# Kernel tuning notes

Hardware: AMD Instinct MI355X
Metric: run time of the kernel (lower is better)

## Reference

```python
import jax, jax.numpy as jnp
import numpy as np

MARGIN = 1.0
EPS = 1e-10


def setup_inputs() -> dict:
    key = jax.random.key(0)
    k1, k2, k3 = jax.random.split(key, 3)
    C, D = 4096, 1024
    B, A = 8, 32
    cls_features = jax.random.normal(k1, (C, D), dtype=jnp.float32)
    prototypes = jax.random.normal(k2, (C, D), dtype=jnp.float32)
    annotations = jax.random.randint(k3, (B, A, 5), 0, C, dtype=jnp.int64)
    return {"cls_features": cls_features, "prototypes": prototypes,
            "annotations": annotations, "steps": 1000}


def reference(cls_features, prototypes, annotations, steps):
    C, D = cls_features.shape
    protos = jax.lax.stop_gradient(prototypes)  # prototypes.detach()

    # one_hot presence of each class in the batch annotations (col 4 = class id, -1 = pad)
    targets = annotations[:, :, 4]                      # [B, A]
    valid = targets != -1
    counts = jnp.zeros((C,), jnp.float32).at[
        jnp.where(valid, targets, 0).ravel()
    ].add(valid.astype(jnp.float32).ravel())
    mask_i = counts > 0                                  # class present in batch
    mask_j = jnp.sum(protos, axis=-1) != 0               # prototypes[j].sum() != 0

    # pairwise mean squared distance: msd[i, j] = mean((feat_i - proto_j)^2)
    f2 = jnp.sum(cls_features * cls_features, axis=-1)   # [C]
    p2 = jnp.sum(protos * protos, axis=-1)               # [C]
    cross = cls_features @ protos.T                      # [C, C]
    msd = jnp.maximum(f2[:, None] + p2[None, :] - 2.0 * cross, 0.0) / D

    pair_mask = mask_i[:, None] & mask_j[None, :]
    eye = jnp.eye(C, dtype=bool)
    intra_mask = pair_mask & eye
    inter_mask = pair_mask & ~eye

    intra_count = jnp.sum(intra_mask.astype(jnp.float32))
    inter_count = jnp.sum(inter_mask.astype(jnp.float32))

    intra_loss = jnp.sum(jnp.where(intra_mask, msd, 0.0)) / (intra_count + EPS)

    s = jnp.sqrt(jnp.maximum(msd, 1e-12))
    e = MARGIN - s
    inter_term = (e / MARGIN) ** 2 * jnp.maximum(e, 0.0) ** 2
    inter_loss = jnp.sum(jnp.where(inter_mask, inter_term, 0.0)) / (inter_count + EPS)

    return (intra_loss, inter_loss)
```

## Files before the change

kernel.cpp:

```cpp
#include <hip/hip_runtime.h>
#include <hip/hip_bf16.h>

typedef float f32x4 __attribute__((ext_vector_type(4)));
typedef int   i32x4 __attribute__((ext_vector_type(4)));
typedef int   i32x8 __attribute__((ext_vector_type(8)));

#define NC 4096
#define ND 1024
#define NVP 256
#define EPSF 1e-10f
#define NT 8
#define SCALE1 127


__global__ void mask_compact_kernel(const int* __restrict__ ann, int n_ann,
                                    float* __restrict__ counts,
                                    int* __restrict__ vidx, int* __restrict__ nv,
                                    float* __restrict__ accum) {
  __shared__ unsigned char mark[NC];
  __shared__ int wsum[4];
  int tid = threadIdx.x;
  for (int i = tid; i < NC; i += 256) mark[i] = 0;
  __syncthreads();
  for (int t = tid; t < n_ann; t += 256) {
    int idx = ann[t * 5 + 4];
    if (idx >= 0 && idx < NC) mark[idx] = 1;
  }
  __syncthreads();
  for (int i = tid; i < NC; i += 256) counts[i] = (float)mark[i];
  int base = tid * 16, lc = 0;
  #pragma unroll
  for (int k = 0; k < 16; ++k) lc += mark[base + k];
  int lane = tid & 63, wid = tid >> 6;
  int inc = lc;
  #pragma unroll
  for (int off = 1; off < 64; off <<= 1) {
    int v = __shfl_up(inc, off);
    if (lane >= off) inc += v;
  }
  if (lane == 63) wsum[wid] = inc;
  __syncthreads();
  int wbase = 0;
  for (int w = 0; w < wid; ++w) wbase += wsum[w];
  int pos = wbase + inc - lc;
  for (int k = 0; k < 16; ++k)
    if (mark[base + k]) vidx[pos++] = base + k;
  int total = wsum[0] + wsum[1] + wsum[2] + wsum[3];
  if (tid == 0) *nv = total;
  for (int i = total + tid; i < NVP; i += 256) vidx[i] = 0;
  if (tid < 8) accum[tid] = 0.f;
}

__global__ void convert_kernel(const float* __restrict__ F, const float* __restrict__ P,
                               unsigned char* __restrict__ Fc, unsigned char* __restrict__ Pb,
                               float* __restrict__ f2c, float* __restrict__ p2,
                               float* __restrict__ psum,
                               const int* __restrict__ vidx, const int* __restrict__ nv) {
  int bid = blockIdx.x;
  int tid = threadIdx.x;
  bool isP = bid < NC;
  float4 v = {0.f, 0.f, 0.f, 0.f};
  int orow = 0;
  if (isP) {
    orow = bid;
    v = *reinterpret_cast<const float4*>(P + (size_t)orow * ND + tid * 4);
  } else {
    int ci = bid - NC;
    orow = ci;
    if (ci < *nv) {
      int row = vidx[ci];
      v = *reinterpret_cast<const float4*>(F + (size_t)row * ND + tid * 4);
    }
  }
  int pk = __builtin_amdgcn_cvt_pk_fp8_f32(v.x, v.y, 0, false);
  pk = __builtin_amdgcn_cvt_pk_fp8_f32(v.z, v.w, pk, true);
  {
    int d0 = tid * 4;
    int kt = d0 >> 7, hi = (d0 >> 5) & 3, half = (d0 >> 4) & 1, b = d0 & 15;
    int R16 = orow >> 4, lo = orow & 15;
    int nr16 = isP ? NC / 16 : NVP / 16;
    unsigned char* dst = isP ? Pb : Fc;
    size_t fa = ((((size_t)kt * nr16 + R16) * 2 + half) * 64 + hi * 16 + lo) * 16 + b;
    *reinterpret_cast<int*>(dst + fa) = pk;
  }
  float sq = v.x * v.x + v.y * v.y + v.z * v.z + v.w * v.w;
  float sm = v.x + v.y + v.z + v.w;
  #pragma unroll
  for (int off = 32; off; off >>= 1) {
    sq += __shfl_down(sq, off);
    sm += __shfl_down(sm, off);
  }
  __shared__ float rs[4], rm[4];
  int wid = tid >> 6, lane = tid & 63;
  if (lane == 0) { rs[wid] = sq; rm[wid] = sm; }
  __syncthreads();
  if (tid == 0) {
    float tsq = rs[0] + rs[1] + rs[2] + rs[3];
    float tsm = rm[0] + rm[1] + rm[2] + rm[3];
    if (isP) { p2[orow] = tsq; psum[orow] = tsm; }
    else     { f2c[orow] = tsq; }
  }
}

#define LDFRAG(V, BASEPTR, FID)                                               \
  do {                                                                        \
    const unsigned char* _p = (BASEPTR) + (size_t)(FID) * 2048 + lane * 16;   \
    i32x4 _l0 = *(const i32x4*)(_p);                                          \
    i32x4 _l1 = *(const i32x4*)(_p + 1024);                                   \
    V = __builtin_shufflevector(_l0, _l1, 0, 1, 2, 3, 4, 5, 6, 7);            \
  } while (0)

#define MFMA4(AV, BV)                                                         \
  do {                                                                        \
    _Pragma("unroll")                                                         \
    for (int _m = 0; _m < 2; ++_m)                                            \
      _Pragma("unroll")                                                       \
      for (int _n = 0; _n < 2; ++_n)                                          \
        acc[_m][_n] = __builtin_amdgcn_mfma_scale_f32_16x16x128_f8f6f4(       \
            AV[_m], BV[_n], acc[_m][_n], 0 , 0 ,            \
            0, SCALE1, 0, SCALE1);                                            \
  } while (0)

__global__ __launch_bounds__(256)
void gemm_loss_kernel(const unsigned char* __restrict__ Fc,
                      const unsigned char* __restrict__ Pb,
                      const float* __restrict__ f2c, const float* __restrict__ p2,
                      const float* __restrict__ psum, const int* __restrict__ vidx,
                      const int* __restrict__ nv, float* __restrict__ accum) {
  __shared__ float redI[4], redE[4];
  const int bi = blockIdx.x >> 6;
  const int bj = blockIdx.x & 63;
  const int tid = threadIdx.x;
  const int lane = tid & 63, wid = tid >> 6;
  const int wr = wid >> 1, wc = wid & 1;
  const int lo = lane & 15, hi = lane >> 4;
  const int ra = bi * 4 + wr * 2;
  const int rb = bj * 4 + wc * 2;

  f32x4 acc[2][2];
  f32x4 zero = {0.f, 0.f, 0.f, 0.f};
  #pragma unroll
  for (int m = 0; m < 2; ++m)
    #pragma unroll
    for (int n = 0; n < 2; ++n) acc[m][n] = zero;

  i32x8 a0[2], b0[2], a1[2], b1[2];
  LDFRAG(a0[0], Fc, 0 * 16 + ra);  LDFRAG(a0[1], Fc, 0 * 16 + ra + 1);
  LDFRAG(b0[0], Pb, 0 * 256 + rb); LDFRAG(b0[1], Pb, 0 * 256 + rb + 1);
  #pragma unroll 1
  for (int kt = 0; kt < NT; kt += 2) {
    LDFRAG(a1[0], Fc, (kt + 1) * 16 + ra);  LDFRAG(a1[1], Fc, (kt + 1) * 16 + ra + 1);
    LDFRAG(b1[0], Pb, (kt + 1) * 256 + rb); LDFRAG(b1[1], Pb, (kt + 1) * 256 + rb + 1);
    MFMA4(a0, b0);
    if (kt + 2 < NT) {
      LDFRAG(a0[0], Fc, (kt + 2) * 16 + ra);  LDFRAG(a0[1], Fc, (kt + 2) * 16 + ra + 1);
      LDFRAG(b0[0], Pb, (kt + 2) * 256 + rb); LDFRAG(b0[1], Pb, (kt + 2) * 256 + rb + 1);
    }
    MFMA4(a1, b1);
  }

  int Nv = *nv;
  float intra_l = 0.f, inter_l = 0.f;
  const int ci0 = bi * 64 + wr * 32 + hi * 4;
  const int gj0 = bj * 64 + wc * 32 + lo;
  #pragma unroll
  for (int n = 0; n < 2; ++n) {
    int gj = gj0 + n * 16;
    float p2j = p2[gj];
    bool mj = psum[gj] != 0.f;
    if (mj) {
      #pragma unroll
      for (int m = 0; m < 2; ++m) {
        #pragma unroll
        for (int r = 0; r < 4; ++r) {
          int ci = ci0 + m * 16 + r;
          if (ci >= Nv) continue;
          float cij = acc[m][n][r];
          float msd = fmaxf(f2c[ci] + p2j - 2.f * cij, 0.f) * (1.f / 1024.f);
          int gi = vidx[ci];
          if (gi == gj) {
            intra_l += msd;
          } else if (msd < 1.0f) {
            float s = sqrtf(fmaxf(msd, 1e-12f));
            float e = 1.f - s;
            float e2 = e * e;
            inter_l += e2 * e2;
          }
        }
      }
    }
  }
  #pragma unroll
  for (int off = 32; off; off >>= 1) {
    intra_l += __shfl_down(intra_l, off);
    inter_l += __shfl_down(inter_l, off);
  }
  if (lane == 0) { redI[wid] = intra_l; redE[wid] = inter_l; }
  __syncthreads();
  if (tid == 0) {
    atomicAdd(&accum[0], redI[0] + redI[1] + redI[2] + redI[3]);
    atomicAdd(&accum[1], redE[0] + redE[1] + redE[2] + redE[3]);
  }
}

__global__ void finalize_kernel(const float* __restrict__ counts,
                                const float* __restrict__ psum,
                                const float* __restrict__ accum,
                                float* __restrict__ out) {
  int tid = threadIdx.x;
  int ni = 0, nj = 0, nd = 0;
  for (int i = tid; i < NC; i += 256) {
    int mi = counts[i] > 0.f;
    int mj = psum[i] != 0.f;
    ni += mi; nj += mj; nd += (mi & mj);
  }
  #pragma unroll
  for (int off = 32; off; off >>= 1) {
    ni += __shfl_down(ni, off);
    nj += __shfl_down(nj, off);
    nd += __shfl_down(nd, off);
  }
  __shared__ int r0[4], r1[4], r2[4];
  int wid = tid >> 6, lane = tid & 63;
  if (lane == 0) { r0[wid] = ni; r1[wid] = nj; r2[wid] = nd; }
  __syncthreads();
  if (tid == 0) {
    float fni = (float)(r0[0] + r0[1] + r0[2] + r0[3]);
    float fnj = (float)(r1[0] + r1[1] + r1[2] + r1[3]);
    float fnd = (float)(r2[0] + r2[1] + r2[2] + r2[3]);
    out[0] = accum[0] / (fnd + EPSF);
    out[1] = accum[1] / (fni * fnj - fnd + EPSF);
  }
}

extern "C" void kernel_launch(void* const* d_in, const int* in_sizes, int n_in,
                              void* d_out, int out_size, void* d_ws, size_t ws_size,
                              hipStream_t stream) {
  const float* F = (const float*)d_in[0];
  const float* P = (const float*)d_in[1];
  const int* ann = (const int*)d_in[2];
  int n_ann = in_sizes[2] / 5;

  char* ws = (char*)d_ws;
  unsigned char* Pb = (unsigned char*)ws;
  unsigned char* Fc = (unsigned char*)(ws + (size_t)NC * ND);
  float* p2     = (float*)(ws + (size_t)NC * ND + (size_t)NVP * ND);
  float* psum   = p2 + NC;
  float* counts = psum + NC;
  float* f2c    = counts + NC;
  float* accum  = f2c + NVP;
  int*   vidx   = (int*)(accum + 8);
  int*   nv     = vidx + NVP;

  float* out = (float*)d_out;

  mask_compact_kernel<<<1, 256, 0, stream>>>(ann, n_ann, counts, vidx, nv, accum);
  convert_kernel<<<NC + NVP, 256, 0, stream>>>(F, P, Fc, Pb, f2c, p2, psum, vidx, nv);
  gemm_loss_kernel<<<4 * 64, 256, 0, stream>>>(Fc, Pb, f2c, p2, psum, vidx, nv, accum);
  finalize_kernel<<<1, 256, 0, stream>>>(counts, psum, accum, out);
}
```

Baseline: 34.56 us.

## Fuse prototype FP8 conversion into GEMM via swizzled LDS and merge mask prep

The separate mask-compaction and conversion kernels become one prep kernel. Sixteen blocks each redo the annotation marking and compaction, then convert their slice of the gathered feature rows to FP8. Prototype rows are no longer staged through a global FP8 buffer: each GEMM block converts its 16 prototype rows directly into XOR-swizzled LDS and computes their norms and sums there. Each block then multiplies against all compacted feature rows. This removes a launch and a global write-and-read pass over the prototypes, at the cost of redundant mask work per prep block and a different GEMM tiling. The finalize step now counts present classes from the compacted indices.

```diff
diff --git a/kernel.cpp b/kernel.cpp
--- a/kernel.cpp
+++ b/kernel.cpp
@@ -9,17 +9,22 @@
 #define ND 1024
 #define NVP 256
 #define EPSF 1e-10f
-#define NT 8
 #define SCALE1 127
 
 
-__global__ void mask_compact_kernel(const int* __restrict__ ann, int n_ann,
-                                    float* __restrict__ counts,
-                                    int* __restrict__ vidx, int* __restrict__ nv,
-                                    float* __restrict__ accum) {
+__global__ __launch_bounds__(256)
+void prep_kernel(const int* __restrict__ ann, int n_ann,
+                 const float* __restrict__ F,
+                 unsigned char* __restrict__ Fc, float* __restrict__ f2c,
+                 int* __restrict__ vidx, int* __restrict__ nv,
+                 float* __restrict__ accum) {
   __shared__ unsigned char mark[NC];
   __shared__ int wsum[4];
-  int tid = threadIdx.x;
+  __shared__ int vloc[NVP];
+  __shared__ float rs[4];
+  const int tid = threadIdx.x;
+  const int lane = tid & 63, wid = tid >> 6;
+
   for (int i = tid; i < NC; i += 256) mark[i] = 0;
   __syncthreads();
   for (int t = tid; t < n_ann; t += 256) {
@@ -27,11 +32,9 @@
     if (idx >= 0 && idx < NC) mark[idx] = 1;
   }
   __syncthreads();
-  for (int i = tid; i < NC; i += 256) counts[i] = (float)mark[i];
   int base = tid * 16, lc = 0;
   #pragma unroll
   for (int k = 0; k < 16; ++k) lc += mark[base + k];
-  int lane = tid & 63, wid = tid >> 6;
   int inc = lc;
   #pragma unroll
   for (int off = 1; off < 64; off <<= 1) {
@@ -44,61 +47,45 @@
   for (int w = 0; w < wid; ++w) wbase += wsum[w];
   int pos = wbase + inc - lc;
   for (int k = 0; k < 16; ++k)
-    if (mark[base + k]) vidx[pos++] = base + k;
-  int total = wsum[0] + wsum[1] + wsum[2] + wsum[3];
-  if (tid == 0) *nv = total;
-  for (int i = total + tid; i < NVP; i += 256) vidx[i] = 0;
-  if (tid < 8) accum[tid] = 0.f;
-}
-
-__global__ void convert_kernel(const float* __restrict__ F, const float* __restrict__ P,
-                               unsigned char* __restrict__ Fc, unsigned char* __restrict__ Pb,
-                               float* __restrict__ f2c, float* __restrict__ p2,
-                               float* __restrict__ psum,
-                               const int* __restrict__ vidx, const int* __restrict__ nv) {
-  int bid = blockIdx.x;
-  int tid = threadIdx.x;
-  bool isP = bid < NC;
-  float4 v = {0.f, 0.f, 0.f, 0.f};
-  int orow = 0;
-  if (isP) {
-    orow = bid;
-    v = *reinterpret_cast<const float4*>(P + (size_t)orow * ND + tid * 4);
-  } else {
-    int ci = bid - NC;
-    orow = ci;
-    if (ci < *nv) {
-      int row = vidx[ci];
-      v = *reinterpret_cast<const float4*>(F + (size_t)row * ND + tid * 4);
-    }
-  }
-  int pk = __builtin_amdgcn_cvt_pk_fp8_f32(v.x, v.y, 0, false);
-  pk = __builtin_amdgcn_cvt_pk_fp8_f32(v.z, v.w, pk, true);
-  {
+    if (mark[base + k]) vloc[pos++] = base + k;
+  const int total = wsum[0] + wsum[1] + wsum[2] + wsum[3];
+  __syncthreads();
+  for (int i = total + tid; i < NVP; i += 256) vloc[i] = 0;
+  __syncthreads();
+
+  if (blockIdx.x == 0) {
+    for (int i = tid; i < NVP; i += 256) vidx[i] = vloc[i];
+    if (tid == 0) *nv = total;
+    if (tid < 8) accum[tid] = 0.f;
+  }
+
+  float4 vv[16];
+  #pragma unroll
+  for (int j = 0; j < 16; ++j) {
+    int slot = blockIdx.x * 16 + j;
+    float4 v = {0.f, 0.f, 0.f, 0.f};
+    if (slot < total)
+      v = *reinterpret_cast<const float4*>(F + (size_t)vloc[slot] * ND + tid * 4);
+    vv[j] = v;
+  }
+  #pragma unroll 1
+  for (int j = 0; j < 16; ++j) {
+    int slot = blockIdx.x * 16 + j;
+    float4 v = vv[j];
+    int pk = __builtin_amdgcn_cvt_pk_fp8_f32(v.x, v.y, 0, false);
+    pk = __builtin_amdgcn_cvt_pk_fp8_f32(v.z, v.w, pk, true);
     int d0 = tid * 4;
-    int kt = d0 >> 7, hi = (d0 >> 5) & 3, half = (d0 >> 4) & 1, b = d0 & 15;
-    int R16 = orow >> 4, lo = orow & 15;
-    int nr16 = isP ? NC / 16 : NVP / 16;
-    unsigned char* dst = isP ? Pb : Fc;
-    size_t fa = ((((size_t)kt * nr16 + R16) * 2 + half) * 64 + hi * 16 + lo) * 16 + b;
-    *reinterpret_cast<int*>(dst + fa) = pk;
-  }
-  float sq = v.x * v.x + v.y * v.y + v.z * v.z + v.w * v.w;
-  float sm = v.x + v.y + v.z + v.w;
-  #pragma unroll
-  for (int off = 32; off; off >>= 1) {
-    sq += __shfl_down(sq, off);
-    sm += __shfl_down(sm, off);
-  }
-  __shared__ float rs[4], rm[4];
-  int wid = tid >> 6, lane = tid & 63;
-  if (lane == 0) { rs[wid] = sq; rm[wid] = sm; }
-  __syncthreads();
-  if (tid == 0) {
-    float tsq = rs[0] + rs[1] + rs[2] + rs[3];
-    float tsm = rm[0] + rm[1] + rm[2] + rm[3];
-    if (isP) { p2[orow] = tsq; psum[orow] = tsm; }
-    else     { f2c[orow] = tsq; }
+    int kt = d0 >> 7, hif = (d0 >> 5) & 3, half = (d0 >> 4) & 1, b = d0 & 15;
+    int R16 = slot >> 4, lof = slot & 15;
+    size_t fa = ((((size_t)kt * 16 + R16) * 2 + half) * 64 + hif * 16 + lof) * 16 + b;
+    *reinterpret_cast<int*>(Fc + fa) = pk;
+    float sq = v.x * v.x + v.y * v.y + v.z * v.z + v.w * v.w;
+    #pragma unroll
+    for (int off = 32; off; off >>= 1) sq += __shfl_down(sq, off);
+    if (lane == 0) rs[wid] = sq;
+    __syncthreads();
+    if (tid == 0) f2c[slot] = rs[0] + rs[1] + rs[2] + rs[3];
+    __syncthreads();
   }
 }
 
@@ -110,73 +97,80 @@
     V = __builtin_shufflevector(_l0, _l1, 0, 1, 2, 3, 4, 5, 6, 7);            \
   } while (0)
 
-#define MFMA4(AV, BV)                                                         \
-  do {                                                                        \
-    _Pragma("unroll")                                                         \
-    for (int _m = 0; _m < 2; ++_m)                                            \
-      _Pragma("unroll")                                                       \
-      for (int _n = 0; _n < 2; ++_n)                                          \
-        acc[_m][_n] = __builtin_amdgcn_mfma_scale_f32_16x16x128_f8f6f4(       \
-            AV[_m], BV[_n], acc[_m][_n], 0 , 0 ,            \
-            0, SCALE1, 0, SCALE1);                                            \
-  } while (0)
-
-__global__ __launch_bounds__(256)
-void gemm_loss_kernel(const unsigned char* __restrict__ Fc,
-                      const unsigned char* __restrict__ Pb,
-                      const float* __restrict__ f2c, const float* __restrict__ p2,
-                      const float* __restrict__ psum, const int* __restrict__ vidx,
-                      const int* __restrict__ nv, float* __restrict__ accum) {
-  __shared__ float redI[4], redE[4];
-  const int bi = blockIdx.x >> 6;
-  const int bj = blockIdx.x & 63;
+__global__ __launch_bounds__(512)
+void pgemm_kernel(const float* __restrict__ P,
+                  const unsigned char* __restrict__ Fc,
+                  const float* __restrict__ f2c,
+                  const int* __restrict__ vidx, const int* __restrict__ nv,
+                  float* __restrict__ psum, float* __restrict__ accum) {
+  __shared__ __attribute__((aligned(16))) unsigned char bfrag[8 * 2048];
+  __shared__ float p2l[16], psl[16], redI[8], redE[8];
   const int tid = threadIdx.x;
   const int lane = tid & 63, wid = tid >> 6;
-  const int wr = wid >> 1, wc = wid & 1;
+  const int bj = blockIdx.x;
+
+  {
+    const int r = tid >> 5;
+    const int seg = tid & 31;
+    const float* src = P + (size_t)(bj * 16 + r) * ND;
+    float sq = 0.f, sm = 0.f;
+    #pragma unroll
+    for (int i = 0; i < 8; ++i) {
+      float4 v = *reinterpret_cast<const float4*>(src + (seg + i * 32) * 4);
+      int pk = __builtin_amdgcn_cvt_pk_fp8_f32(v.x, v.y, 0, false);
+      pk = __builtin_amdgcn_cvt_pk_fp8_f32(v.z, v.w, pk, true);
+      int addr = i * 2048 + r * 128 + ((seg * 4) ^ ((r & 7) << 4));
+      *reinterpret_cast<int*>(&bfrag[addr]) = pk;
+      sq += v.x * v.x + v.y * v.y + v.z * v.z + v.w * v.w;
+      sm += v.x + v.y + v.z + v.w;
+    }
+    #pragma unroll
+    for (int off = 16; off; off >>= 1) {
+      sq += __shfl_down(sq, off, 32);
+      sm += __shfl_down(sm, off, 32);
+    }
+    if ((tid & 31) == 0) {
+      p2l[r] = sq; psl[r] = sm;
+      psum[bj * 16 + r] = sm;
+    }
+  }
+  __syncthreads();
+
   const int lo = lane & 15, hi = lane >> 4;
-  const int ra = bi * 4 + wr * 2;
-  const int rb = bj * 4 + wc * 2;
-
-  f32x4 acc[2][2];
-  f32x4 zero = {0.f, 0.f, 0.f, 0.f};
-  #pragma unroll
-  for (int m = 0; m < 2; ++m)
-    #pragma unroll
-    for (int n = 0; n < 2; ++n) acc[m][n] = zero;
-
-  i32x8 a0[2], b0[2], a1[2], b1[2];
-  LDFRAG(a0[0], Fc, 0 * 16 + ra);  LDFRAG(a0[1], Fc, 0 * 16 + ra + 1);
-  LDFRAG(b0[0], Pb, 0 * 256 + rb); LDFRAG(b0[1], Pb, 0 * 256 + rb + 1);
-  #pragma unroll 1
-  for (int kt = 0; kt < NT; kt += 2) {
-    LDFRAG(a1[0], Fc, (kt + 1) * 16 + ra);  LDFRAG(a1[1], Fc, (kt + 1) * 16 + ra + 1);
-    LDFRAG(b1[0], Pb, (kt + 1) * 256 + rb); LDFRAG(b1[1], Pb, (kt + 1) * 256 + rb + 1);
-    MFMA4(a0, b0);
-    if (kt + 2 < NT) {
-      LDFRAG(a0[0], Fc, (kt + 2) * 16 + ra);  LDFRAG(a0[1], Fc, (kt + 2) * 16 + ra + 1);
-      LDFRAG(b0[0], Pb, (kt + 2) * 256 + rb); LDFRAG(b0[1], Pb, (kt + 2) * 256 + rb + 1);
-    }
-    MFMA4(a1, b1);
+  f32x4 acc0 = {0.f, 0.f, 0.f, 0.f}, acc1 = acc0;
+  const int fbase = wid * 2;
+  #pragma unroll 4
+  for (int kt = 0; kt < 8; ++kt) {
+    i32x8 a0, a1, b;
+    LDFRAG(a0, Fc, kt * 16 + fbase);
+    LDFRAG(a1, Fc, kt * 16 + fbase + 1);
+    {
+      int x = (lo & 7) << 4;
+      const unsigned char* bb = &bfrag[kt * 2048 + lo * 128];
+      i32x4 l0 = *reinterpret_cast<const i32x4*>(bb + ((hi * 32) ^ x));
+      i32x4 l1 = *reinterpret_cast<const i32x4*>(bb + ((hi * 32 + 16) ^ x));
+      b = __builtin_shufflevector(l0, l1, 0, 1, 2, 3, 4, 5, 6, 7);
+    }
+    acc0 = __builtin_amdgcn_mfma_scale_f32_16x16x128_f8f6f4(
+        a0, b, acc0, 0, 0, 0, SCALE1, 0, SCALE1);
+    acc1 = __builtin_amdgcn_mfma_scale_f32_16x16x128_f8f6f4(
+        a1, b, acc1, 0, 0, 0, SCALE1, 0, SCALE1);
   }
 
   int Nv = *nv;
   float intra_l = 0.f, inter_l = 0.f;
-  const int ci0 = bi * 64 + wr * 32 + hi * 4;
-  const int gj0 = bj * 64 + wc * 32 + lo;
-  #pragma unroll
-  for (int n = 0; n < 2; ++n) {
-    int gj = gj0 + n * 16;
-    float p2j = p2[gj];
-    bool mj = psum[gj] != 0.f;
-    if (mj) {
+  const int gj = bj * 16 + lo;
+  const float p2j = p2l[lo];
+  const bool mj = psl[lo] != 0.f;
+  if (mj) {
+    #pragma unroll
+    for (int f = 0; f < 2; ++f) {
+      f32x4 a = f ? acc1 : acc0;
       #pragma unroll
-      for (int m = 0; m < 2; ++m) {
-        #pragma unroll
-        for (int r = 0; r < 4; ++r) {
-          int ci = ci0 + m * 16 + r;
-          if (ci >= Nv) continue;
-          float cij = acc[m][n][r];
-          float msd = fmaxf(f2c[ci] + p2j - 2.f * cij, 0.f) * (1.f / 1024.f);
+      for (int r = 0; r < 4; ++r) {
+        int ci = wid * 32 + f * 16 + hi * 4 + r;
+        if (ci < Nv) {
+          float msd = fmaxf(f2c[ci] + p2j - 2.f * a[r], 0.f) * (1.f / 1024.f);
           int gi = vidx[ci];
           if (gi == gj) {
             intra_l += msd;
@@ -198,34 +192,35 @@
   if (lane == 0) { redI[wid] = intra_l; redE[wid] = inter_l; }
   __syncthreads();
   if (tid == 0) {
-    atomicAdd(&accum[0], redI[0] + redI[1] + redI[2] + redI[3]);
-    atomicAdd(&accum[1], redE[0] + redE[1] + redE[2] + redE[3]);
-  }
-}
-
-__global__ void finalize_kernel(const float* __restrict__ counts,
-                                const float* __restrict__ psum,
+    float si = 0.f, se = 0.f;
+    #pragma unroll
+    for (int w = 0; w < 8; ++w) { si += redI[w]; se += redE[w]; }
+    atomicAdd(&accum[0], si);
+    atomicAdd(&accum[1], se);
+  }
+}
+
+__global__ void finalize_kernel(const float* __restrict__ psum,
+                                const int* __restrict__ vidx,
+                                const int* __restrict__ nv,
                                 const float* __restrict__ accum,
                                 float* __restrict__ out) {
+  __shared__ int r1[4], r2[4];
   int tid = threadIdx.x;
-  int ni = 0, nj = 0, nd = 0;
-  for (int i = tid; i < NC; i += 256) {
-    int mi = counts[i] > 0.f;
-    int mj = psum[i] != 0.f;
-    ni += mi; nj += mj; nd += (mi & mj);
-  }
+  int Nv = *nv;
+  int nj = 0, nd = 0;
+  for (int i = tid; i < NC; i += 256) nj += (psum[i] != 0.f);
+  for (int c = tid; c < Nv; c += 256) nd += (psum[vidx[c]] != 0.f);
   #pragma unroll
   for (int off = 32; off; off >>= 1) {
-    ni += __shfl_down(ni, off);
     nj += __shfl_down(nj, off);
     nd += __shfl_down(nd, off);
   }
-  __shared__ int r0[4], r1[4], r2[4];
   int wid = tid >> 6, lane = tid & 63;
-  if (lane == 0) { r0[wid] = ni; r1[wid] = nj; r2[wid] = nd; }
+  if (lane == 0) { r1[wid] = nj; r2[wid] = nd; }
   __syncthreads();
   if (tid == 0) {
-    float fni = (float)(r0[0] + r0[1] + r0[2] + r0[3]);
+    float fni = (float)Nv;
     float fnj = (float)(r1[0] + r1[1] + r1[2] + r1[3]);
     float fnd = (float)(r2[0] + r2[1] + r2[2] + r2[3]);
     out[0] = accum[0] / (fnd + EPSF);
@@ -242,20 +237,16 @@
   int n_ann = in_sizes[2] / 5;
 
   char* ws = (char*)d_ws;
-  unsigned char* Pb = (unsigned char*)ws;
-  unsigned char* Fc = (unsigned char*)(ws + (size_t)NC * ND);
-  float* p2     = (float*)(ws + (size_t)NC * ND + (size_t)NVP * ND);
-  float* psum   = p2 + NC;
-  float* counts = psum + NC;
-  float* f2c    = counts + NC;
-  float* accum  = f2c + NVP;
-  int*   vidx   = (int*)(accum + 8);
-  int*   nv     = vidx + NVP;
+  unsigned char* Fc = (unsigned char*)ws;
+  float* f2c   = (float*)(ws + (size_t)NVP * ND);
+  float* psum  = f2c + NVP;
+  float* accum = psum + NC;
+  int*   vidx  = (int*)(accum + 8);
+  int*   nv    = vidx + NVP;
 
   float* out = (float*)d_out;
 
-  mask_compact_kernel<<<1, 256, 0, stream>>>(ann, n_ann, counts, vidx, nv, accum);
-  convert_kernel<<<NC + NVP, 256, 0, stream>>>(F, P, Fc, Pb, f2c, p2, psum, vidx, nv);
-  gemm_loss_kernel<<<4 * 64, 256, 0, stream>>>(Fc, Pb, f2c, p2, psum, vidx, nv, accum);
-  finalize_kernel<<<1, 256, 0, stream>>>(counts, psum, accum, out);
-}
+  prep_kernel<<<NVP / 16, 256, 0, stream>>>(ann, n_ann, F, Fc, f2c, vidx, nv, accum);
+  pgemm_kernel<<<NC / 16, 512, 0, stream>>>(P, Fc, f2c, vidx, nv, psum, accum);
+  finalize_kernel<<<1, 256, 0, stream>>>(psum, vidx, nv, accum, out);
+}
```

New measurement: 43.35 us. +25.4%, slower.
